# Optimization experiments

Measured on AMD Instinct MI355X. Metric: run time of the kernel, lower is better.

Reference implementation:

```python
import jax, jax.numpy as jnp
import numpy as np
from jax import lax

B, S, T = 32, 100, 4
NUM_C2, NUM_C3, NUM_D, DV = 500, 2000, 1000, 128


def setup_inputs():
    key = jax.random.key(0)
    ks = jax.random.split(key, 25)
    s = 0.05
    def nrm(k, shape):
        return jax.random.normal(k, shape, dtype=jnp.float32) * s
    return {
        "c2_seq": jax.random.randint(ks[0], (B, S), 0, NUM_C2),
        "c3_seq": jax.random.randint(ks[1], (B, S, T), 1, NUM_C3 + 1),  # 0 is padding; use all-valid tags
        "d_seq": jax.random.randint(ks[2], (B, S), 0, NUM_D),
        "r_seq": jax.random.randint(ks[3], (B, S), 0, 2),
        "D_emb": nrm(ks[4], (NUM_D, 1)),
        "R_emb": nrm(ks[5], (2, DV)),
        "v_c2": nrm(ks[6], (DV,)),
        "v_c3": nrm(ks[7], (DV,)),
        "v_d": nrm(ks[8], (DV,)),
        "W_ih": nrm(ks[9], (3 * DV, 2 * DV)),
        "W_hh": nrm(ks[10], (3 * DV, DV)),
        "b_ih": nrm(ks[11], (3 * DV,)),
        "b_hh": nrm(ks[12], (3 * DV,)),
        "l1_W1": nrm(ks[13], (DV, DV)), "l1_b1": nrm(ks[14], (DV,)),
        "l1_W2": nrm(ks[15], (1, DV)), "l1_b2": nrm(ks[16], (1,)),
        "l2_W1": nrm(ks[17], (DV, 4 * DV)), "l2_b1": nrm(ks[18], (DV,)),
        "l2_W2": nrm(ks[19], (1, DV)), "l2_b2": nrm(ks[20], (1,)),
        "l3_W1": nrm(ks[21], (DV, 4 * DV)), "l3_b1": nrm(ks[22], (DV,)),
        "l3_W2": nrm(ks[23], (1, DV)), "l3_b2": nrm(ks[24], (1,)),
    }


def _mlp(x, W1, b1, W2, b2):
    # Linear -> ReLU -> (Dropout: identity in eval) -> Linear -> (Dropout)
    return jnp.maximum(x @ W1.T + b1, 0.0) @ W2.T + b2


def _gru(x_seq, h0, W_ih, W_hh, b_ih, b_hh):
    # torch.nn.GRU math, batch_first
    def step(h, x):
        gi = x @ W_ih.T + b_ih
        gh = h @ W_hh.T + b_hh
        i_r, i_z, i_n = jnp.split(gi, 3, axis=-1)
        h_r, h_z, h_n = jnp.split(gh, 3, axis=-1)
        r = jax.nn.sigmoid(i_r + h_r)
        z = jax.nn.sigmoid(i_z + h_z)
        n = jnp.tanh(i_n + r * h_n)
        h_new = (1.0 - z) * n + z * h
        return h_new, h_new
    _, hs = lax.scan(step, h0, jnp.swapaxes(x_seq, 0, 1))
    return jnp.swapaxes(hs, 0, 1)


def _forward(c2_seq, c3_seq, d_seq, r_seq, p):
    (D_emb, R_emb, v_c2, v_c3, v_d, W_ih, W_hh, b_ih, b_hh,
     l1_W1, l1_b1, l1_W2, l1_b2, l2_W1, l2_b1, l2_W2, l2_b2,
     l3_W1, l3_b1, l3_W2, l3_b2) = p
    Bn = c2_seq.shape[0]
    gamma = D_emb[d_seq]                      # [B,S,1]
    v_d_seq = gamma * v_d                     # [B,S,DV]
    v_r_seq = R_emb[r_seq]                    # [B,S,DV]
    h0 = jnp.zeros((Bn, DV), dtype=v_d_seq.dtype)
    h_seq = _gru(jnp.concatenate([v_d_seq, v_r_seq], -1), h0, W_ih, W_hh, b_ih, b_hh)
    alpha_seq = _mlp(h_seq, l1_W1, l1_b1, l1_W2, l1_b2)[..., 0]   # [B,S]

    def step(carry, xs):
        C2, C3 = carry
        c2, c3, vd, vr = xs                                      # [B],[B,T],[B,DV],[B,DV]
        mask = (c3 != 0).astype(C3.dtype)                        # [B,T]
        w = mask / mask.sum(-1, keepdims=True)
        beta2 = jnp.take_along_axis(C2, c2[:, None], axis=-1)    # [B,1]
        beta3 = jnp.take_along_axis(C3, c3, axis=-1)             # [B,T]
        beta3_bar = (beta3 * w).sum(-1)                          # [B]
        vc2 = beta2 * v_c2                                       # [B,DV]
        vc3 = beta3[..., None] * v_c3                            # [B,T,DV]
        vc3_bar = beta3_bar[:, None] * v_c3                      # [B,DV]
        new_c2 = _mlp(jnp.concatenate([vc2, vc3_bar, vd, vr], -1),
                      l2_W1, l2_b1, l2_W2, l2_b2)[:, 0]          # [B]
        feat3 = jnp.concatenate([
            jnp.broadcast_to(vc2[:, None, :], vc3.shape), vc3,
            jnp.broadcast_to(vd[:, None, :], vc3.shape),
            jnp.broadcast_to(vr[:, None, :], vc3.shape)], -1)    # [B,T,4*DV]
        new_c3 = _mlp(feat3, l3_W1, l3_b1, l3_W2, l3_b2)[..., 0]  # [B,T]
        oh2 = jax.nn.one_hot(c2, NUM_C2, dtype=C2.dtype)          # [B,NC2]
        oh3 = jax.nn.one_hot(c3, NUM_C3 + 1, dtype=C3.dtype) * mask[..., None]  # [B,T,NC3+1]
        multi = oh3.sum(1)
        C2n = C2 * (1.0 - oh2) + new_c2[:, None] * oh2
        C3n = C3 * (1.0 - multi) + (new_c3[..., None] * oh3).sum(1)
        return (C2n, C3n), (C2n, C3n)

    C2_0 = jnp.zeros((Bn, NUM_C2), dtype=jnp.float32)
    C3_0 = jnp.zeros((Bn, NUM_C3 + 1), dtype=jnp.float32)
    xs = (jnp.swapaxes(c2_seq, 0, 1), jnp.swapaxes(c3_seq, 0, 1),
          jnp.swapaxes(v_d_seq, 0, 1), jnp.swapaxes(v_r_seq, 0, 1))
    _, (C2_seq, C3_seq) = lax.scan(step, (C2_0, C3_0), xs)
    C2_seq = jnp.swapaxes(C2_seq, 0, 1)   # [B,S,NUM_C2]
    C3_seq = jnp.swapaxes(C3_seq, 0, 1)   # [B,S,NUM_C3+1]
    return alpha_seq, h_seq, C2_seq, C3_seq


def reference(c2_seq, c3_seq, d_seq, r_seq, D_emb, R_emb, v_c2, v_c3, v_d,
              W_ih, W_hh, b_ih, b_hh, l1_W1, l1_b1, l1_W2, l1_b2,
              l2_W1, l2_b1, l2_W2, l2_b2, l3_W1, l3_b1, l3_W2, l3_b2):
    p = (D_emb, R_emb, v_c2, v_c3, v_d, W_ih, W_hh, b_ih, b_hh,
         l1_W1, l1_b1, l1_W2, l1_b2, l2_W1, l2_b1, l2_W2, l2_b2,
         l3_W1, l3_b1, l3_W2, l3_b2)
    return _forward(c2_seq, c3_seq, d_seq, r_seq, p)
```

## Files before the change

### kernel.cpp

```cpp
#include <hip/hip_runtime.h>

#define BB   32
#define SS   100
#define TT   4
#define NCC2 500
#define NC3P 2001
#define DD   128

#define HALL 3456
#define LDSF 16256

__device__ __forceinline__ float fast_rcp(float x) { return __builtin_amdgcn_rcpf(x); }
__device__ __forceinline__ float fast_sig(float x) { return fast_rcp(1.f + __expf(-x)); }
__device__ __forceinline__ float fast_tanh(float x) { return 1.f - 2.f * fast_rcp(__expf(2.f * x) + 1.f); }

__device__ __forceinline__ float dpp_sum64(float x) {
    x += __int_as_float(__builtin_amdgcn_update_dpp(0, __float_as_int(x), 0x111, 0xf, 0xf, true));
    x += __int_as_float(__builtin_amdgcn_update_dpp(0, __float_as_int(x), 0x112, 0xf, 0xf, true));
    x += __int_as_float(__builtin_amdgcn_update_dpp(0, __float_as_int(x), 0x114, 0xf, 0xf, true));
    x += __int_as_float(__builtin_amdgcn_update_dpp(0, __float_as_int(x), 0x118, 0xf, 0xf, true));
    x += __int_as_float(__builtin_amdgcn_update_dpp(0, __float_as_int(x), 0x142, 0xa, 0xf, true));
    x += __int_as_float(__builtin_amdgcn_update_dpp(0, __float_as_int(x), 0x143, 0xc, 0xf, true));
    return x;
}

__device__ __forceinline__ float dpp_sum16(float x) {
    x += __int_as_float(__builtin_amdgcn_update_dpp(0, __float_as_int(x), 0x111, 0xf, 0xf, true));
    x += __int_as_float(__builtin_amdgcn_update_dpp(0, __float_as_int(x), 0x112, 0xf, 0xf, true));
    x += __int_as_float(__builtin_amdgcn_update_dpp(0, __float_as_int(x), 0x114, 0xf, 0xf, true));
    x += __int_as_float(__builtin_amdgcn_update_dpp(0, __float_as_int(x), 0x118, 0xf, 0xf, true));
    return x;
}

__device__ __forceinline__ float dot4(float4 a, float4 b) {
    return fmaf(a.x, b.x, fmaf(a.y, b.y, fmaf(a.z, b.z, a.w * b.w)));
}

#define FMA4(W, H) do { a0 = fmaf((W).x, (H).x, a0); a1 = fmaf((W).y, (H).y, a1); \
                        a2 = fmaf((W).z, (H).z, a2); a3 = fmaf((W).w, (H).w, a3); } while (0)

__global__ __launch_bounds__(64) void k_pre(const float* __restrict__ l2W1,
                                            const float* __restrict__ l3W1,
                                            const float* __restrict__ v_c2,
                                            const float* __restrict__ v_c3,
                                            const float* __restrict__ v_d,
                                            const float* __restrict__ Remb,
                                            float* __restrict__ ws)
{
    const int t = threadIdx.x;
    const int g = t >> 4;
    const int c = (t & 15) * 8;
    const float* vsrc = (g == 0) ? v_c2 : (g == 1) ? v_c3 : (g == 2) ? v_d : Remb;
    const float4 va  = *(const float4*)(vsrc + c);
    const float4 vb  = *(const float4*)(vsrc + c + 4);
    const float4 va1 = *(const float4*)(Remb + 128 + c);
    const float4 vb1 = *(const float4*)(Remb + 132 + c);
#pragma unroll
    for (int r = 0; r < 8; ++r) {
        const int row_id = blockIdx.x * 8 + r;
        const float* W = (row_id < 128) ? l2W1 : l3W1;
        float* U = ws + ((row_id < 128) ? 0 : 640);
        const int i = row_id & 127;
        const float* wr = W + i * 512 + g * 128 + c;
        const float4 w0 = *(const float4*)(wr);
        const float4 w1 = *(const float4*)(wr + 4);
        float p  = dot4(w0, va)  + dot4(w1, vb);
        float p1 = dot4(w0, va1) + dot4(w1, vb1);
        p  = dpp_sum16(p);
        p1 = dpp_sum16(p1);
        if ((t & 15) == 15) {
            U[g * 128 + i] = p;
            if (g == 3) U[512 + i] = p1;
        }
    }
}

__global__ __launch_bounds__(768, 1) void k_main(
    const int* __restrict__ c2_seq, const int* __restrict__ c3_seq,
    const int* __restrict__ d_seq,  const int* __restrict__ r_seq,
    const float* __restrict__ D_emb, const float* __restrict__ Remb,
    const float* __restrict__ v_d,
    const float* __restrict__ W_ih, const float* __restrict__ W_hh,
    const float* __restrict__ b_ih, const float* __restrict__ b_hh,
    const float* __restrict__ l2b1, const float* __restrict__ l2W2, const float* __restrict__ l2b2,
    const float* __restrict__ l3b1, const float* __restrict__ l3W2, const float* __restrict__ l3b2,
    const float* __restrict__ ws, float* __restrict__ h_out,
    float* __restrict__ C2o, float* __restrict__ C3o)
{
    __shared__ __align__(16) float sh[LDSF];
    int* shi = (int*)sh;
    const int blk = blockIdx.x;
    const int t = threadIdx.x;

    if (blk < BB) {
        const int b = blk;
        const int p = (t >= 384) ? 1 : 0;
        const int j = t - p * 384;
        const float4* wrow = reinterpret_cast<const float4*>(W_hh + j * DD + p * 64);
        const float4 w0 = wrow[0],  w1 = wrow[1],  w2 = wrow[2],  w3 = wrow[3];
        const float4 w4 = wrow[4],  w5 = wrow[5],  w6 = wrow[6],  w7 = wrow[7];
        const float4 w8 = wrow[8],  w9 = wrow[9],  w10 = wrow[10], w11 = wrow[11];
        const float4 w12 = wrow[12], w13 = wrow[13], w14 = wrow[14], w15 = wrow[15];

        float pd = 0.f, pr0 = 0.f, pr1 = 0.f;
        {
            const float4* wd4 = (const float4*)(W_ih + j * 256 + p * 64);
            const float4* wr4 = (const float4*)(W_ih + j * 256 + 128 + p * 64);
            const float4* vd4 = (const float4*)(v_d + p * 64);
            const float4* r04 = (const float4*)(Remb + p * 64);
            const float4* r14 = (const float4*)(Remb + 128 + p * 64);
#pragma unroll
            for (int k4 = 0; k4 < 16; ++k4) {
                const float4 wd = wd4[k4], wr = wr4[k4];
                const float4 vd = vd4[k4], r0 = r04[k4], r1 = r14[k4];
                pd  = fmaf(wd.x, vd.x, fmaf(wd.y, vd.y, fmaf(wd.z, vd.z, fmaf(wd.w, vd.w, pd))));
                pr0 = fmaf(wr.x, r0.x, fmaf(wr.y, r0.y, fmaf(wr.z, r0.z, fmaf(wr.w, r0.w, pr0))));
                pr1 = fmaf(wr.x, r1.x, fmaf(wr.y, r1.y, fmaf(wr.z, r1.z, fmaf(wr.w, r1.w, pr1))));
            }
        }
        sh[896 + t] = pd; sh[1664 + t] = pr0; sh[2432 + t] = pr1;
        if (t < DD) sh[t] = 0.f;
        if (t < SS) {
            sh[3200 + t]  = D_emb[d_seq[b * SS + t]];
            shi[3300 + t] = r_seq[b * SS + t];
        }
        __syncthreads();

        float gd_r=0,gd_z=0,gd_n=0, g0_r=0,g0_z=0,g0_n=0, g1_r=0,g1_z=0,g1_n=0;
        float bi_r=0,bi_z=0,bi_n=0, bh_r=0,bh_z=0,bh_n=0, h = 0.f;
        if (t < DD) {
            gd_r = sh[896+t]      + sh[896+t+384];
            gd_z = sh[896+t+128]  + sh[896+t+512];
            gd_n = sh[896+t+256]  + sh[896+t+640];
            g0_r = sh[1664+t]     + sh[1664+t+384];
            g0_z = sh[1664+t+128] + sh[1664+t+512];
            g0_n = sh[1664+t+256] + sh[1664+t+640];
            g1_r = sh[2432+t]     + sh[2432+t+384];
            g1_z = sh[2432+t+128] + sh[2432+t+512];
            g1_n = sh[2432+t+256] + sh[2432+t+640];
            bi_r = b_ih[t]; bi_z = b_ih[t+128]; bi_n = b_ih[t+256];
            bh_r = b_hh[t]; bh_z = b_hh[t+128]; bh_n = b_hh[t+256];
        }
        __syncthreads();

        for (int s = 0; s < SS; ++s) {
            float a0 = 0.f, a1 = 0.f, a2 = 0.f, a3 = 0.f;
            const float4* hv4 = reinterpret_cast<const float4*>(sh) + p * 16;
            float4 h0 = hv4[0], h1 = hv4[1], h2 = hv4[2], h3 = hv4[3];
            FMA4(w0, h0); FMA4(w1, h1); FMA4(w2, h2); FMA4(w3, h3);
            h0 = hv4[4]; h1 = hv4[5]; h2 = hv4[6]; h3 = hv4[7];
            FMA4(w4, h0); FMA4(w5, h1); FMA4(w6, h2); FMA4(w7, h3);
            h0 = hv4[8]; h1 = hv4[9]; h2 = hv4[10]; h3 = hv4[11];
            FMA4(w8, h0); FMA4(w9, h1); FMA4(w10, h2); FMA4(w11, h3);
            h0 = hv4[12]; h1 = hv4[13]; h2 = hv4[14]; h3 = hv4[15];
            FMA4(w12, h0); FMA4(w13, h1); FMA4(w14, h2); FMA4(w15, h3);
            sh[128 + t] = (a0 + a1) + (a2 + a3);
            __syncthreads();
            if (t < DD) {
                float ghr = sh[128+t]     + sh[128+t+384] + bh_r;
                float ghz = sh[128+t+128] + sh[128+t+512] + bh_z;
                float ghn = sh[128+t+256] + sh[128+t+640] + bh_n;
                float gamma = sh[3200 + s]; int rr = shi[3300 + s];
                float gir = fmaf(gamma, gd_r, (rr ? g1_r : g0_r) + bi_r);
                float giz = fmaf(gamma, gd_z, (rr ? g1_z : g0_z) + bi_z);
                float gin = fmaf(gamma, gd_n, (rr ? g1_n : g0_n) + bi_n);
                float r = fast_sig(gir + ghr);
                float z = fast_sig(giz + ghz);
                float n = fast_tanh(fmaf(r, ghn, gin));
                h = (1.f - z) * n + z * h;
                sh[t] = h;
                sh[HALL + s * DD + t] = h;
            }
            __syncthreads();
        }

        {
            const float4* hsrc = reinterpret_cast<const float4*>(sh + HALL);
            float4* hdst = reinterpret_cast<float4*>(h_out + (size_t)b * SS * DD);
            for (int i = t; i < SS * DD / 4; i += 768) hdst[i] = hsrc[i];
        }
    } else if (t < 64) {
        const int b = blk - BB;
        float* C2s = sh;
        float* C3s = sh + NCC2;
        for (int k = t; k < NCC2 + NC3P; k += 64) sh[k] = 0.f;
        for (int k = t; k < SS; k += 64) {
            shi[2501 + k] = c2_seq[b * SS + k];
            sh[3004 + k]  = D_emb[d_seq[b * SS + k]];
            shi[3104 + k] = r_seq[b * SS + k];
        }
        for (int k = t; k < SS; k += 64)
            reinterpret_cast<int4*>(shi + 2604)[k] = reinterpret_cast<const int4*>(c3_seq + b * SS * TT)[k];

        const float* u2 = ws;
        const float* u3 = ws + 640;
        const float u2a0 = u2[t],        u2a1 = u2[64 + t];
        const float u2b0 = u2[128 + t],  u2b1 = u2[192 + t];
        const float u2c0 = u2[256 + t],  u2c1 = u2[320 + t];
        const float u2d00 = u2[384 + t], u2d01 = u2[448 + t];
        const float u2d10 = u2[512 + t], u2d11 = u2[576 + t];
        const float u3a0 = u3[t],        u3a1 = u3[64 + t];
        const float u3b0 = u3[128 + t],  u3b1 = u3[192 + t];
        const float u3c0 = u3[256 + t],  u3c1 = u3[320 + t];
        const float u3d00 = u3[384 + t], u3d01 = u3[448 + t];
        const float u3d10 = u3[512 + t], u3d11 = u3[576 + t];
        const float b2_0 = l2b1[t], b2_1 = l2b1[64 + t];
        const float w2_0 = l2W2[t], w2_1 = l2W2[64 + t];
        const float b3_0 = l3b1[t], b3_1 = l3b1[64 + t];
        const float w3_0 = l3W2[t], w3_1 = l3W2[64 + t];
        const float c2bias = l2b2[0], c3bias = l3b2[0];

        int  nc2 = shi[2501];
        int4 nc3 = reinterpret_cast<const int4*>(shi + 2604)[0];
        float ngam = sh[3004];
        int   nrr  = shi[3104];

        for (int s = 0; s < SS; ++s) {
            const int rs = b * SS + s;
            const int c2i = nc2;
            const int i0 = nc3.x, i1 = nc3.y, i2 = nc3.z, i3 = nc3.w;
            const float gamma = ngam;
            const int rr = nrr;
            if (s + 1 < SS) {
                nc2 = shi[2501 + s + 1];
                nc3 = reinterpret_cast<const int4*>(shi + 2604)[s + 1];
                ngam = sh[3004 + s + 1];
                nrr  = shi[3104 + s + 1];
            }

            const float beta2 = C2s[c2i];
            const bool k0 = (i0 != 0), k1 = (i1 != 0), k2 = (i2 != 0), k3 = (i3 != 0);
            const float m0 = k0 ? 1.f : 0.f, m1 = k1 ? 1.f : 0.f;
            const float m2 = k2 ? 1.f : 0.f, m3 = k3 ? 1.f : 0.f;
            const float bt0 = C3s[i0], bt1 = C3s[i1], bt2 = C3s[i2], bt3 = C3s[i3];
            const float msum = m0 + m1 + m2 + m3;
            const float b3bar = (bt0 * m0 + bt1 * m1 + bt2 * m2 + bt3 * m3) * fast_rcp(msum);

            const float ud20 = rr ? u2d10 : u2d00, ud21 = rr ? u2d11 : u2d01;
            const float ud30 = rr ? u3d10 : u3d00, ud31 = rr ? u3d11 : u3d01;

            float h20 = fmaf(beta2, u2a0, fmaf(b3bar, u2b0, fmaf(gamma, u2c0, ud20 + b2_0)));
            float h21 = fmaf(beta2, u2a1, fmaf(b3bar, u2b1, fmaf(gamma, u2c1, ud21 + b2_1)));
            float newc2 = dpp_sum64(fmaf(fmaxf(h20, 0.f), w2_0, fmaxf(h21, 0.f) * w2_1)) + c2bias;

            const float base30 = fmaf(beta2, u3a0, fmaf(gamma, u3c0, ud30 + b3_0));
            const float base31 = fmaf(beta2, u3a1, fmaf(gamma, u3c1, ud31 + b3_1));
            float ha, hb, q0, q1, q2, q3;
            ha = fmaf(bt0, u3b0, base30); hb = fmaf(bt0, u3b1, base31);
            q0 = dpp_sum64(fmaf(fmaxf(ha, 0.f), w3_0, fmaxf(hb, 0.f) * w3_1)) + c3bias;
            ha = fmaf(bt1, u3b0, base30); hb = fmaf(bt1, u3b1, base31);
            q1 = dpp_sum64(fmaf(fmaxf(ha, 0.f), w3_0, fmaxf(hb, 0.f) * w3_1)) + c3bias;
            ha = fmaf(bt2, u3b0, base30); hb = fmaf(bt2, u3b1, base31);
            q2 = dpp_sum64(fmaf(fmaxf(ha, 0.f), w3_0, fmaxf(hb, 0.f) * w3_1)) + c3bias;
            ha = fmaf(bt3, u3b0, base30); hb = fmaf(bt3, u3b1, base31);
            q3 = dpp_sum64(fmaf(fmaxf(ha, 0.f), w3_0, fmaxf(hb, 0.f) * w3_1)) + c3bias;

            float val0, val1, val2, val3;
            {
                float c = m0 + ((k1 && i1 == i0) ? 1.f : 0.f) + ((k2 && i2 == i0) ? 1.f : 0.f) + ((k3 && i3 == i0) ? 1.f : 0.f);
                float qs = (k0 ? q0 : 0.f) + ((k1 && i1 == i0) ? q1 : 0.f) + ((k2 && i2 == i0) ? q2 : 0.f) + ((k3 && i3 == i0) ? q3 : 0.f);
                val0 = bt0 * (1.f - c) + qs;
            }
            {
                float c = ((k0 && i0 == i1) ? 1.f : 0.f) + m1 + ((k2 && i2 == i1) ? 1.f : 0.f) + ((k3 && i3 == i1) ? 1.f : 0.f);
                float qs = ((k0 && i0 == i1) ? q0 : 0.f) + (k1 ? q1 : 0.f) + ((k2 && i2 == i1) ? q2 : 0.f) + ((k3 && i3 == i1) ? q3 : 0.f);
                val1 = bt1 * (1.f - c) + qs;
            }
            {
                float c = ((k0 && i0 == i2) ? 1.f : 0.f) + ((k1 && i1 == i2) ? 1.f : 0.f) + m2 + ((k3 && i3 == i2) ? 1.f : 0.f);
                float qs = ((k0 && i0 == i2) ? q0 : 0.f) + ((k1 && i1 == i2) ? q1 : 0.f) + (k2 ? q2 : 0.f) + ((k3 && i3 == i2) ? q3 : 0.f);
                val2 = bt2 * (1.f - c) + qs;
            }
            {
                float c = ((k0 && i0 == i3) ? 1.f : 0.f) + ((k1 && i1 == i3) ? 1.f : 0.f) + ((k2 && i2 == i3) ? 1.f : 0.f) + m3;
                float qs = ((k0 && i0 == i3) ? q0 : 0.f) + ((k1 && i1 == i3) ? q1 : 0.f) + ((k2 && i2 == i3) ? q2 : 0.f) + (k3 ? q3 : 0.f);
                val3 = bt3 * (1.f - c) + qs;
            }

            if (t == 63) {
                C2s[c2i] = newc2;
                if (k0) C3s[i0] = val0;
                if (k1) C3s[i1] = val1;
                if (k2) C3s[i2] = val2;
                if (k3) C3s[i3] = val3;
            }

            float* c2row = C2o + (size_t)rs * NCC2;
            float* c3row = C3o + (size_t)rs * NC3P;
            *reinterpret_cast<float4*>(c2row + 4 * t) = *reinterpret_cast<const float4*>(C2s + 4 * t);
            if (t < 61)
                *reinterpret_cast<float4*>(c2row + 256 + 4 * t) = *reinterpret_cast<const float4*>(C2s + 256 + 4 * t);
            const int p0 = (4 - (rs & 3)) & 3;
            if (p0 == 0) {
#pragma unroll
                for (int i = 0; i < 8; ++i) {
                    int d4 = i * 64 + t;
                    if (d4 < 500)
                        reinterpret_cast<float4*>(c3row)[d4] = reinterpret_cast<const float4*>(C3s)[d4];
                }
                if (t == 0) c3row[2000] = C3s[2000];
            } else {
                const int tail = (2001 - p0) & 3;
                const int dt = 2001 - tail;
                if (t < p0) c3row[t] = C3s[t];
                if (t < tail) c3row[dt + t] = C3s[dt + t];
#pragma unroll
                for (int i = 0; i < 8; ++i) {
                    int d = p0 + 4 * (i * 64 + t);
                    if (d + 3 <= 2000) {
                        float4 v;
                        v.x = C3s[d]; v.y = C3s[d + 1]; v.z = C3s[d + 2]; v.w = C3s[d + 3];
                        *reinterpret_cast<float4*>(c3row + d) = v;
                    }
                }
            }
        }
    }
}

__global__ __launch_bounds__(256) void k_alpha2(const float* __restrict__ h_seq,
                                                const float* __restrict__ W1,
                                                const float* __restrict__ b1,
                                                const float* __restrict__ W2,
                                                const float* __restrict__ b2,
                                                float* __restrict__ alpha)
{
    __shared__ float part[256];
    __shared__ float red[2];
    const int t = threadIdx.x;
    const int ch = t & 127, half = t >> 7;
    const float4* w4 = (const float4*)(W1 + ch * 128 + half * 64);
    float4 w[16];
#pragma unroll
    for (int i = 0; i < 16; ++i) w[i] = w4[i];
    const float b1v = b1[ch];
    const float w2v = W2[ch];
    const float b2v = b2[0];
    const int base = blockIdx.x * 16;
    for (int r = 0; r < 16; ++r) {
        const float* h = h_seq + (size_t)(base + r) * 128 + half * 64;
        float a0 = 0.f, a1 = 0.f, a2 = 0.f, a3 = 0.f;
#pragma unroll
        for (int i = 0; i < 16; ++i) {
            float4 hv = *(const float4*)(h + 4 * i);
            a0 = fmaf(w[i].x, hv.x, a0); a1 = fmaf(w[i].y, hv.y, a1);
            a2 = fmaf(w[i].z, hv.z, a2); a3 = fmaf(w[i].w, hv.w, a3);
        }
        part[t] = (a0 + a1) + (a2 + a3);
        __syncthreads();
        if (t < 128) {
            float v = fmaxf(part[t] + part[t + 128] + b1v, 0.f) * w2v;
            v = dpp_sum64(v);
            if ((t & 63) == 63) red[t >> 6] = v;
        }
        __syncthreads();
        if (t == 0) alpha[base + r] = red[0] + red[1] + b2v;
    }
}

extern "C" void kernel_launch(void* const* d_in, const int* in_sizes, int n_in,
                              void* d_out, int out_size, void* d_ws, size_t ws_size,
                              hipStream_t stream)
{
    (void)in_sizes; (void)n_in; (void)out_size; (void)ws_size;
    const int*   c2_seq = (const int*)d_in[0];
    const int*   c3_seq = (const int*)d_in[1];
    const int*   d_seq  = (const int*)d_in[2];
    const int*   r_seq  = (const int*)d_in[3];
    const float* D_emb  = (const float*)d_in[4];
    const float* Remb   = (const float*)d_in[5];
    const float* v_c2   = (const float*)d_in[6];
    const float* v_c3   = (const float*)d_in[7];
    const float* v_d    = (const float*)d_in[8];
    const float* W_ih   = (const float*)d_in[9];
    const float* W_hh   = (const float*)d_in[10];
    const float* b_ih   = (const float*)d_in[11];
    const float* b_hh   = (const float*)d_in[12];
    const float* l1W1   = (const float*)d_in[13];
    const float* l1b1   = (const float*)d_in[14];
    const float* l1W2   = (const float*)d_in[15];
    const float* l1b2   = (const float*)d_in[16];
    const float* l2W1   = (const float*)d_in[17];
    const float* l2b1   = (const float*)d_in[18];
    const float* l2W2   = (const float*)d_in[19];
    const float* l2b2   = (const float*)d_in[20];
    const float* l3W1   = (const float*)d_in[21];
    const float* l3b1   = (const float*)d_in[22];
    const float* l3W2   = (const float*)d_in[23];
    const float* l3b2   = (const float*)d_in[24];

    float* out   = (float*)d_out;
    float* alpha = out;
    float* h_out = out + 3200;
    float* C2o   = out + 412800;
    float* C3o   = out + 2012800;
    float* ws    = (float*)d_ws;

    k_pre<<<32, 64, 0, stream>>>(l2W1, l3W1, v_c2, v_c3, v_d, Remb, ws);
    k_main<<<2 * BB, 768, 0, stream>>>(c2_seq, c3_seq, d_seq, r_seq, D_emb, Remb, v_d,
                                       W_ih, W_hh, b_ih, b_hh,
                                       l2b1, l2W2, l2b2, l3b1, l3W2, l3b2,
                                       ws, h_out, C2o, C3o);
    k_alpha2<<<200, 256, 0, stream>>>(h_out, l1W1, l1b1, l1W2, l1b2, alpha);
}
```

Before: 129.0 us.

## Stage GRU weights as fp16 in LDS, split C-row writes across blocks, retile alpha MLP

```diff
diff --git a/kernel.cpp b/kernel.cpp
--- a/kernel.cpp
+++ b/kernel.cpp
@@ -7,8 +7,11 @@
 #define NC3P 2001
 #define DD   128
 
-#define HALL 3456
-#define LDSF 16256
+#define WB    1152
+#define HALLN 25728
+#define LDSF  38528
+
+typedef _Float16 h2v __attribute__((ext_vector_type(2)));
 
 __device__ __forceinline__ float fast_rcp(float x) { return __builtin_amdgcn_rcpf(x); }
 __device__ __forceinline__ float fast_sig(float x) { return fast_rcp(1.f + __expf(-x)); }
@@ -35,9 +38,6 @@
 __device__ __forceinline__ float dot4(float4 a, float4 b) {
     return fmaf(a.x, b.x, fmaf(a.y, b.y, fmaf(a.z, b.z, a.w * b.w)));
 }
-
-#define FMA4(W, H) do { a0 = fmaf((W).x, (H).x, a0); a1 = fmaf((W).y, (H).y, a1); \
-                        a2 = fmaf((W).z, (H).z, a2); a3 = fmaf((W).w, (H).w, a3); } while (0)
 
 __global__ __launch_bounds__(64) void k_pre(const float* __restrict__ l2W1,
                                             const float* __restrict__ l3W1,
@@ -93,14 +93,27 @@
     const int t = threadIdx.x;
 
     if (blk < BB) {
-        const int b = blk;
-        const int p = (t >= 384) ? 1 : 0;
-        const int j = t - p * 384;
-        const float4* wrow = reinterpret_cast<const float4*>(W_hh + j * DD + p * 64);
-        const float4 w0 = wrow[0],  w1 = wrow[1],  w2 = wrow[2],  w3 = wrow[3];
-        const float4 w4 = wrow[4],  w5 = wrow[5],  w6 = wrow[6],  w7 = wrow[7];
-        const float4 w8 = wrow[8],  w9 = wrow[9],  w10 = wrow[10], w11 = wrow[11];
-        const float4 w12 = wrow[12], w13 = wrow[13], w14 = wrow[14], w15 = wrow[15];
+        const int b  = blk;
+        const int wv = t >> 6;
+        const int l  = t & 63;
+        const int p  = (t >= 384) ? 1 : 0;
+        const int j  = t - p * 384;
+        const int p16 = p * 16;
+
+        uint4* wl = reinterpret_cast<uint4*>(sh + WB);
+        {
+            const float4* wr4 = (const float4*)(W_hh + j * DD + p * 64);
+#pragma unroll
+            for (int i = 0; i < 8; ++i) {
+                float4 A = wr4[2 * i], B = wr4[2 * i + 1];
+                uint4 u;
+                u.x = __builtin_bit_cast(unsigned int, __builtin_amdgcn_cvt_pkrtz(A.x, A.y));
+                u.y = __builtin_bit_cast(unsigned int, __builtin_amdgcn_cvt_pkrtz(A.z, A.w));
+                u.z = __builtin_bit_cast(unsigned int, __builtin_amdgcn_cvt_pkrtz(B.x, B.y));
+                u.w = __builtin_bit_cast(unsigned int, __builtin_amdgcn_cvt_pkrtz(B.z, B.w));
+                wl[(wv * 8 + i) * 64 + l] = u;
+            }
+        }
 
         float pd = 0.f, pr0 = 0.f, pr1 = 0.f;
         {
@@ -118,49 +131,56 @@
                 pr1 = fmaf(wr.x, r1.x, fmaf(wr.y, r1.y, fmaf(wr.z, r1.z, fmaf(wr.w, r1.w, pr1))));
             }
         }
-        sh[896 + t] = pd; sh[1664 + t] = pr0; sh[2432 + t] = pr1;
+        sh[HALLN + t] = pd; sh[HALLN + 768 + t] = pr0; sh[HALLN + 1536 + t] = pr1;
         if (t < DD) sh[t] = 0.f;
         if (t < SS) {
-            sh[3200 + t]  = D_emb[d_seq[b * SS + t]];
-            shi[3300 + t] = r_seq[b * SS + t];
+            sh[896 + t]  = D_emb[d_seq[b * SS + t]];
+            shi[996 + t] = r_seq[b * SS + t];
         }
         __syncthreads();
 
         float gd_r=0,gd_z=0,gd_n=0, g0_r=0,g0_z=0,g0_n=0, g1_r=0,g1_z=0,g1_n=0;
         float bi_r=0,bi_z=0,bi_n=0, bh_r=0,bh_z=0,bh_n=0, h = 0.f;
         if (t < DD) {
-            gd_r = sh[896+t]      + sh[896+t+384];
-            gd_z = sh[896+t+128]  + sh[896+t+512];
-            gd_n = sh[896+t+256]  + sh[896+t+640];
-            g0_r = sh[1664+t]     + sh[1664+t+384];
-            g0_z = sh[1664+t+128] + sh[1664+t+512];
-            g0_n = sh[1664+t+256] + sh[1664+t+640];
-            g1_r = sh[2432+t]     + sh[2432+t+384];
-            g1_z = sh[2432+t+128] + sh[2432+t+512];
-            g1_n = sh[2432+t+256] + sh[2432+t+640];
+            gd_r = sh[HALLN+t]        + sh[HALLN+t+384];
+            gd_z = sh[HALLN+t+128]    + sh[HALLN+t+512];
+            gd_n = sh[HALLN+t+256]    + sh[HALLN+t+640];
+            g0_r = sh[HALLN+768+t]     + sh[HALLN+768+t+384];
+            g0_z = sh[HALLN+768+t+128] + sh[HALLN+768+t+512];
+            g0_n = sh[HALLN+768+t+256] + sh[HALLN+768+t+640];
+            g1_r = sh[HALLN+1536+t]     + sh[HALLN+1536+t+384];
+            g1_z = sh[HALLN+1536+t+128] + sh[HALLN+1536+t+512];
+            g1_n = sh[HALLN+1536+t+256] + sh[HALLN+1536+t+640];
             bi_r = b_ih[t]; bi_z = b_ih[t+128]; bi_n = b_ih[t+256];
             bh_r = b_hh[t]; bh_z = b_hh[t+128]; bh_n = b_hh[t+256];
         }
         __syncthreads();
 
+        const uint4* wlr = wl;
         for (int s = 0; s < SS; ++s) {
             float a0 = 0.f, a1 = 0.f, a2 = 0.f, a3 = 0.f;
-            const float4* hv4 = reinterpret_cast<const float4*>(sh) + p * 16;
-            float4 h0 = hv4[0], h1 = hv4[1], h2 = hv4[2], h3 = hv4[3];
-            FMA4(w0, h0); FMA4(w1, h1); FMA4(w2, h2); FMA4(w3, h3);
-            h0 = hv4[4]; h1 = hv4[5]; h2 = hv4[6]; h3 = hv4[7];
-            FMA4(w4, h0); FMA4(w5, h1); FMA4(w6, h2); FMA4(w7, h3);
-            h0 = hv4[8]; h1 = hv4[9]; h2 = hv4[10]; h3 = hv4[11];
-            FMA4(w8, h0); FMA4(w9, h1); FMA4(w10, h2); FMA4(w11, h3);
-            h0 = hv4[12]; h1 = hv4[13]; h2 = hv4[14]; h3 = hv4[15];
-            FMA4(w12, h0); FMA4(w13, h1); FMA4(w14, h2); FMA4(w15, h3);
+            const float4* hv4 = reinterpret_cast<const float4*>(sh);
+#pragma unroll
+            for (int i = 0; i < 8; ++i) {
+                uint4 q = wlr[(wv * 8 + i) * 64 + l];
+                float4 ha = hv4[p16 + 2 * i];
+                float4 hb = hv4[p16 + 2 * i + 1];
+                h2v w01 = __builtin_bit_cast(h2v, q.x);
+                h2v w23 = __builtin_bit_cast(h2v, q.y);
+                h2v w45 = __builtin_bit_cast(h2v, q.z);
+                h2v w67 = __builtin_bit_cast(h2v, q.w);
+                a0 = fmaf((float)w01.x, ha.x, a0); a1 = fmaf((float)w01.y, ha.y, a1);
+                a2 = fmaf((float)w23.x, ha.z, a2); a3 = fmaf((float)w23.y, ha.w, a3);
+                a0 = fmaf((float)w45.x, hb.x, a0); a1 = fmaf((float)w45.y, hb.y, a1);
+                a2 = fmaf((float)w67.x, hb.z, a2); a3 = fmaf((float)w67.y, hb.w, a3);
+            }
             sh[128 + t] = (a0 + a1) + (a2 + a3);
             __syncthreads();
             if (t < DD) {
                 float ghr = sh[128+t]     + sh[128+t+384] + bh_r;
                 float ghz = sh[128+t+128] + sh[128+t+512] + bh_z;
                 float ghn = sh[128+t+256] + sh[128+t+640] + bh_n;
-                float gamma = sh[3200 + s]; int rr = shi[3300 + s];
+                float gamma = sh[896 + s]; int rr = shi[996 + s];
                 float gir = fmaf(gamma, gd_r, (rr ? g1_r : g0_r) + bi_r);
                 float giz = fmaf(gamma, gd_z, (rr ? g1_z : g0_z) + bi_z);
                 float gin = fmaf(gamma, gd_n, (rr ? g1_n : g0_n) + bi_n);
@@ -169,18 +189,19 @@
                 float n = fast_tanh(fmaf(r, ghn, gin));
                 h = (1.f - z) * n + z * h;
                 sh[t] = h;
-                sh[HALL + s * DD + t] = h;
+                sh[HALLN + s * DD + t] = h;
             }
             __syncthreads();
         }
 
         {
-            const float4* hsrc = reinterpret_cast<const float4*>(sh + HALL);
+            const float4* hsrc = reinterpret_cast<const float4*>(sh + HALLN);
             float4* hdst = reinterpret_cast<float4*>(h_out + (size_t)b * SS * DD);
             for (int i = t; i < SS * DD / 4; i += 768) hdst[i] = hsrc[i];
         }
     } else if (t < 64) {
-        const int b = blk - BB;
+        const int b = (blk - BB) >> 2;
+        const int q = (blk - BB) & 3;
         float* C2s = sh;
         float* C3s = sh + NCC2;
         for (int k = t; k < NCC2 + NC3P; k += 64) sh[k] = 0.f;
@@ -285,77 +306,87 @@
                 if (k3) C3s[i3] = val3;
             }
 
-            float* c2row = C2o + (size_t)rs * NCC2;
-            float* c3row = C3o + (size_t)rs * NC3P;
-            *reinterpret_cast<float4*>(c2row + 4 * t) = *reinterpret_cast<const float4*>(C2s + 4 * t);
-            if (t < 61)
-                *reinterpret_cast<float4*>(c2row + 256 + 4 * t) = *reinterpret_cast<const float4*>(C2s + 256 + 4 * t);
-            const int p0 = (4 - (rs & 3)) & 3;
-            if (p0 == 0) {
-#pragma unroll
-                for (int i = 0; i < 8; ++i) {
-                    int d4 = i * 64 + t;
-                    if (d4 < 500)
-                        reinterpret_cast<float4*>(c3row)[d4] = reinterpret_cast<const float4*>(C3s)[d4];
+            if (q == 0) {
+                float* c2row = C2o + (size_t)rs * NCC2;
+                const float4* src = reinterpret_cast<const float4*>(C2s);
+                float4* dst = reinterpret_cast<float4*>(c2row);
+                dst[t] = src[t];
+                if (t < 61) dst[64 + t] = src[64 + t];
+            } else {
+                float* c3row = C3o + (size_t)rs * NC3P;
+                const int lo = (q - 1) * 667;
+                const int n = 667;
+                int pre = (4 - (int)(((unsigned)(rs * NC3P + lo)) & 3)) & 3;
+                if (pre > n) pre = n;
+                if (t < pre) c3row[lo + t] = C3s[lo + t];
+                const int st = lo + pre;
+                const int rem = n - pre;
+                const int nv = rem >> 2, tl = rem & 3;
+                for (int i = t; i < nv; i += 64) {
+                    const int d = st + 4 * i;
+                    *reinterpret_cast<float4*>(c3row + d) =
+                        make_float4(C3s[d], C3s[d + 1], C3s[d + 2], C3s[d + 3]);
                 }
-                if (t == 0) c3row[2000] = C3s[2000];
-            } else {
-                const int tail = (2001 - p0) & 3;
-                const int dt = 2001 - tail;
-                if (t < p0) c3row[t] = C3s[t];
-                if (t < tail) c3row[dt + t] = C3s[dt + t];
-#pragma unroll
-                for (int i = 0; i < 8; ++i) {
-                    int d = p0 + 4 * (i * 64 + t);
-                    if (d + 3 <= 2000) {
-                        float4 v;
-                        v.x = C3s[d]; v.y = C3s[d + 1]; v.z = C3s[d + 2]; v.w = C3s[d + 3];
-                        *reinterpret_cast<float4*>(c3row + d) = v;
-                    }
+                if (t < tl) {
+                    const int d = st + 4 * nv + t;
+                    c3row[d] = C3s[d];
                 }
             }
         }
     }
 }
 
-__global__ __launch_bounds__(256) void k_alpha2(const float* __restrict__ h_seq,
-                                                const float* __restrict__ W1,
-                                                const float* __restrict__ b1,
-                                                const float* __restrict__ W2,
-                                                const float* __restrict__ b2,
-                                                float* __restrict__ alpha)
+__global__ __launch_bounds__(256) void k_alpha(const float* __restrict__ h_seq,
+                                               const float* __restrict__ W1,
+                                               const float* __restrict__ b1,
+                                               const float* __restrict__ W2,
+                                               const float* __restrict__ b2,
+                                               float* __restrict__ alpha)
 {
-    __shared__ float part[256];
-    __shared__ float red[2];
+    __shared__ __align__(16) float sl[22560];
     const int t = threadIdx.x;
+    const int base = blockIdx.x * 16;
+
+    float4* hl4 = reinterpret_cast<float4*>(sl);
+    const float4* hg = reinterpret_cast<const float4*>(h_seq + (size_t)base * DD);
+    for (int i = t; i < 512; i += 256) hl4[i] = hg[i];
+
+    float4* wl4 = reinterpret_cast<float4*>(sl + 6144);
+    const float4* wg = reinterpret_cast<const float4*>(W1);
+    for (int g = t; g < 4096; g += 256) {
+        const int ch = g >> 5, k4 = g & 31;
+        wl4[ch * 32 + (k4 ^ (ch & 31))] = wg[g];
+    }
+    __syncthreads();
+
     const int ch = t & 127, half = t >> 7;
-    const float4* w4 = (const float4*)(W1 + ch * 128 + half * 64);
-    float4 w[16];
-#pragma unroll
-    for (int i = 0; i < 16; ++i) w[i] = w4[i];
-    const float b1v = b1[ch];
-    const float w2v = W2[ch];
-    const float b2v = b2[0];
-    const int base = blockIdx.x * 16;
-    for (int r = 0; r < 16; ++r) {
-        const float* h = h_seq + (size_t)(base + r) * 128 + half * 64;
-        float a0 = 0.f, a1 = 0.f, a2 = 0.f, a3 = 0.f;
-#pragma unroll
-        for (int i = 0; i < 16; ++i) {
-            float4 hv = *(const float4*)(h + 4 * i);
-            a0 = fmaf(w[i].x, hv.x, a0); a1 = fmaf(w[i].y, hv.y, a1);
-            a2 = fmaf(w[i].z, hv.z, a2); a3 = fmaf(w[i].w, hv.w, a3);
-        }
-        part[t] = (a0 + a1) + (a2 + a3);
-        __syncthreads();
-        if (t < 128) {
-            float v = fmaxf(part[t] + part[t + 128] + b1v, 0.f) * w2v;
+    float acc[16];
+#pragma unroll
+    for (int r = 0; r < 16; ++r) acc[r] = 0.f;
+#pragma unroll
+    for (int kk = 0; kk < 16; ++kk) {
+        const int k4 = half * 16 + kk;
+        const float4 w = wl4[ch * 32 + (k4 ^ (ch & 31))];
+#pragma unroll
+        for (int r = 0; r < 16; ++r) {
+            const float4 hv = hl4[r * 32 + k4];
+            acc[r] = fmaf(w.x, hv.x, fmaf(w.y, hv.y, fmaf(w.z, hv.z, fmaf(w.w, hv.w, acc[r]))));
+        }
+    }
+#pragma unroll
+    for (int r = 0; r < 16; ++r) sl[2048 + r * 256 + t] = acc[r];
+    __syncthreads();
+    if (t < 128) {
+        const float b1v = b1[t], w2v = W2[t];
+#pragma unroll
+        for (int r = 0; r < 16; ++r) {
+            float v = fmaxf(sl[2048 + r * 256 + t] + sl[2048 + r * 256 + 128 + t] + b1v, 0.f) * w2v;
             v = dpp_sum64(v);
-            if ((t & 63) == 63) red[t >> 6] = v;
-        }
-        __syncthreads();
-        if (t == 0) alpha[base + r] = red[0] + red[1] + b2v;
+            if ((t & 63) == 63) sl[22528 + r * 2 + (t >> 6)] = v;
+        }
     }
+    __syncthreads();
+    if (t < 16) alpha[base + t] = sl[22528 + 2 * t] + sl[22528 + 2 * t + 1] + b2[0];
 }
 
 extern "C" void kernel_launch(void* const* d_in, const int* in_sizes, int n_in,
@@ -397,9 +428,9 @@
     float* ws    = (float*)d_ws;
 
     k_pre<<<32, 64, 0, stream>>>(l2W1, l3W1, v_c2, v_c3, v_d, Remb, ws);
-    k_main<<<2 * BB, 768, 0, stream>>>(c2_seq, c3_seq, d_seq, r_seq, D_emb, Remb, v_d,
-                                       W_ih, W_hh, b_ih, b_hh,
-                                       l2b1, l2W2, l2b2, l3b1, l3W2, l3b2,
-                                       ws, h_out, C2o, C3o);
-    k_alpha2<<<200, 256, 0, stream>>>(h_out, l1W1, l1b1, l1W2, l1b2, alpha);
-}
+    k_main<<<BB + 4 * BB, 768, 0, stream>>>(c2_seq, c3_seq, d_seq, r_seq, D_emb, Remb, v_d,
+                                            W_ih, W_hh, b_ih, b_hh,
+                                            l2b1, l2W2, l2b2, l3b1, l3W2, l3b2,
+                                            ws, h_out, C2o, C3o);
+    k_alpha<<<200, 256, 0, stream>>>(h_out, l1W1, l1b1, l1W2, l1b2, alpha);
+}
```

Result: slower. 150.3 us (+16.6%).
